# Optimization experiments

Hardware: AMD Instinct MI355X
Metric: run time of the kernel (lower is better)

Reference implementation:

```python
import jax, jax.numpy as jnp
import numpy as np

SEQ, B, V, E, H, L, S_SRC = 128, 32, 32000, 1024, 1024, 3, 64


def setup_inputs() -> dict:
    key = jax.random.key(0)
    ks = jax.random.split(key, 8)
    sc = 0.05
    return {
        "tokens": jax.random.randint(ks[0], (SEQ, B), 0, V),
        "emb_W": jax.random.normal(ks[1], (V, E), jnp.float32) * 0.1,
        "W_ih": jax.random.normal(ks[2], (L, 4 * H, E), jnp.float32) * sc,
        "W_hh": jax.random.normal(ks[3], (L, 4 * H, H), jnp.float32) * sc,
        "b_ih": jnp.zeros((L, 4 * H), jnp.float32),
        "b_hh": jnp.zeros((L, 4 * H), jnp.float32),
        "attn_Win": jax.random.normal(ks[4], (E, E), jnp.float32) * sc,
        "attn_Wout": jax.random.normal(ks[5], (E, 2 * E), jnp.float32) * sc,
        "final_b": jnp.zeros((V,), jnp.float32),
        "encoder_outs": jax.random.normal(ks[6], (S_SRC, B, E), jnp.float32),
        "h0": jnp.zeros((L, B, H), jnp.float32),
        "c0": jnp.zeros((L, B, H), jnp.float32),
    }


def reference(tokens, emb_W, W_ih, W_hh, b_ih, b_hh, attn_Win, attn_Wout,
              final_b, encoder_outs, h0, c0):
    # Eval mode: all dropouts (dropoute/i/h/out) are identity.
    emb = emb_W[tokens]                                  # [SEQ, B, E]
    ctx = jnp.transpose(encoder_outs, (1, 0, 2))         # [B, S_src, E]

    def lstm_cell(x, h, c, l):
        gates = x @ W_ih[l].T + b_ih[l] + h @ W_hh[l].T + b_hh[l]  # [B, 4H]
        i, f, g, o = jnp.split(gates, 4, axis=-1)        # torch order: i,f,g,o
        i, f, o = jax.nn.sigmoid(i), jax.nn.sigmoid(f), jax.nn.sigmoid(o)
        g = jnp.tanh(g)
        c_new = f * c + i * g
        return o * jnp.tanh(c_new), c_new

    def step(carry, x_t):
        h, c = carry                                     # each [L, B, H]
        hs, cs = [], []
        inp = x_t
        for l in range(L):
            h_new, c_new = lstm_cell(inp, h[l], c[l], l)
            hs.append(h_new)
            cs.append(c_new)
            inp = h_new                                  # dropouth is identity
        # SoftDotAttention on last layer hidden
        target = h_new @ attn_Win.T                      # [B, E]
        attn = jax.nn.softmax(jnp.einsum('bse,be->bs', ctx, target), axis=-1)
        wc = jnp.einsum('bs,bse->be', attn, ctx)         # weighted context
        h_tilde = jnp.tanh(jnp.concatenate([wc, h_new], axis=-1) @ attn_Wout.T)
        return (jnp.stack(hs), jnp.stack(cs)), h_tilde

    (_, _), outs = jax.lax.scan(step, (h0, c0), emb)     # outs: [SEQ, B, E]
    logits = outs @ emb_W.T + final_b                    # tied weights: [SEQ, B, V]
    return logits
```

## Files before the change

kernel.cpp:

```cpp
#include <hip/hip_runtime.h>
#include <cstdint>
#include <cstddef>

#define SEQ   128
#define BB    32
#define EE    1024
#define HH    1024
#define G4    4096
#define VV    32000
#define NROWS 4096

typedef _Float16 h16x8 __attribute__((ext_vector_type(8)));
typedef _Float16 h16x4 __attribute__((ext_vector_type(4)));
typedef float f32x4  __attribute__((ext_vector_type(4)));

#define AS_G(p) ((const __attribute__((address_space(1))) void*)(p))
#define AS_L(p) ((__attribute__((address_space(3))) void*)(p))

__device__ __forceinline__ float sigmf(float x) { return 1.0f / (1.0f + expf(-x)); }

#define OFF_SYNC    0ull
#define OFF_HFRAG   33024ull
#define OFF_EMB     426240ull
#define OFF_X0      8814848ull
#define OFF_WIH0    42369280ull
#define OFF_WP4     50757888ull
#define OFF_WP0     84312320ull
#define OFF_EMBW    92700928ull
#define OFF_WIN     158236928ull
#define OFF_WOUT    160334080ull
#define OFF_ENC     164528384ull
#define OFF_H2ALL   168722688ull
#define OFF_CONCAT  177111296ull
#define OFF_TARGET  193888512ull
#define OFF_HT      202277120ull
#define WS_NEEDED   210665728ull

__global__ __launch_bounds__(256) void k_conv(const float* __restrict__ s,
                                              _Float16* __restrict__ d, int n4) {
  int i = blockIdx.x * blockDim.x + threadIdx.x;
  int st = gridDim.x * blockDim.x;
  for (; i < n4; i += st) {
    float4 v = ((const float4*)s)[i];
    h16x4 o; o[0] = (_Float16)v.x; o[1] = (_Float16)v.y; o[2] = (_Float16)v.z; o[3] = (_Float16)v.w;
    ((h16x4*)d)[i] = o;
  }
}

__global__ __launch_bounds__(256) void k_gather(const int* __restrict__ tok,
                                                const float* __restrict__ embW,
                                                _Float16* __restrict__ emb) {
  int row = blockIdx.x;
  int t = tok[row];
  float4 v = ((const float4*)(embW + (size_t)t * EE))[threadIdx.x];
  h16x4 o; o[0] = (_Float16)v.x; o[1] = (_Float16)v.y; o[2] = (_Float16)v.z; o[3] = (_Float16)v.w;
  ((h16x4*)(emb + (size_t)row * EE))[threadIdx.x] = o;
}

__global__ __launch_bounds__(256) void k_packw4(const float* __restrict__ Wih,
                                                const float* __restrict__ Whh,
                                                _Float16* __restrict__ out) {
  int i = blockIdx.x * blockDim.x + threadIdx.x;
  int st = gridDim.x * blockDim.x;
  const int total = 256 * 65536;
  for (; i < total; i += st) {
    int w = i >> 16, rem = i & 65535;
    int mat = rem >> 14, jj = (rem >> 10) & 15, k = rem & 1023;
    int layer = 1 + (mat >> 1), isHH = mat & 1;
    int row = ((jj >> 2) << 10) + (w << 2) + (jj & 3);
    int ks = k ^ ((jj & 7) << 3);
    const float* src = (isHH ? Whh : Wih) + (size_t)layer * G4 * 1024 + (size_t)row * 1024 + ks;
    out[i] = (_Float16)(*src);
  }
}

__global__ __launch_bounds__(256) void k_packw0(const float* __restrict__ Whh,
                                                _Float16* __restrict__ out) {
  int i = blockIdx.x * blockDim.x + threadIdx.x;
  int st = gridDim.x * blockDim.x;
  const int total = 256 * 16384;
  for (; i < total; i += st) {
    int w = i >> 14, rem = i & 16383;
    int ks = rem >> 9, lane = (rem >> 3) & 63, e = rem & 7;
    int jj = lane & 15, q = lane >> 4;
    int row = ((jj >> 2) << 10) + (w << 2) + (jj & 3);
    int k = ks * 32 + q * 8 + e;
    out[i] = (_Float16)Whh[(size_t)row * 1024 + k];
  }
}

__global__ __launch_bounds__(256) void k_init(const float* __restrict__ h0,
                                              _Float16* __restrict__ hfrag,
                                              unsigned* __restrict__ sync) {
  int i = blockIdx.x * blockDim.x + threadIdx.x;
  if (i < 64 + 8192) sync[i] = 0u;
  if (i >= 3 * BB * HH) return;
  int l = i >> 15, rem = i & 32767;
  int b = rem >> 10, n = rem & 1023;
  int parI = (l == 1) ? 0 : 1;
  int tbb = b >> 4, ks = n >> 5, q = (n >> 3) & 3, e = n & 7;
  int lane2 = (b & 15) | (q << 4);
  hfrag[(size_t)(l * 2 + parI) * 32768 + ((size_t)(tbb * 32 + ks) * 64 + lane2) * 8 + e] =
      (_Float16)h0[i];
}

template <int EPI>
__global__ __launch_bounds__(256) void k_gemm(const _Float16* __restrict__ A,
                                              const _Float16* __restrict__ B,
                                              void* __restrict__ C, int M, int N, int K,
                                              const float* __restrict__ bias1,
                                              const float* __restrict__ bias2) {
  __shared__ _Float16 As[2][128 * 32];
  __shared__ _Float16 Bs[2][128 * 32];
  const int ntn = N / 128;
  const int tm = blockIdx.x / ntn, tn = blockIdx.x % ntn;
  const int tid = threadIdx.x, lane = tid & 63;
  const int wv = tid >> 6, wr = wv >> 1, wc = wv & 1;
  f32x4 acc[4][4] = {};

  auto stage = [&](int buf, int k0) {
#pragma unroll
    for (int i = 0; i < 2; ++i) {
      int eo = (i * 256 + tid) * 8;
      int r = eo >> 5, c = eo & 31;
      __builtin_amdgcn_global_load_lds(AS_G(A + (size_t)(tm * 128 + r) * K + k0 + c),
                                       AS_L(&As[buf][eo]), 16, 0, 0);
      __builtin_amdgcn_global_load_lds(AS_G(B + (size_t)(tn * 128 + r) * K + k0 + c),
                                       AS_L(&Bs[buf][eo]), 16, 0, 0);
    }
  };
  stage(0, 0);
  __syncthreads();
  const int nk = K / 32;
  for (int kt = 0; kt < nk; ++kt) {
    if (kt + 1 < nk) stage((kt + 1) & 1, (kt + 1) * 32);
    const int buf = kt & 1;
    h16x8 af[4], bfr[4];
#pragma unroll
    for (int mi = 0; mi < 4; ++mi)
      af[mi] = *(const h16x8*)&As[buf][(wr * 64 + mi * 16 + (lane & 15)) * 32 + (lane >> 4) * 8];
#pragma unroll
    for (int ni = 0; ni < 4; ++ni)
      bfr[ni] = *(const h16x8*)&Bs[buf][(wc * 64 + ni * 16 + (lane & 15)) * 32 + (lane >> 4) * 8];
#pragma unroll
    for (int mi = 0; mi < 4; ++mi)
#pragma unroll
      for (int ni = 0; ni < 4; ++ni)
        acc[mi][ni] = __builtin_amdgcn_mfma_f32_16x16x32_f16(af[mi], bfr[ni], acc[mi][ni], 0, 0, 0);
    __syncthreads();
  }
  const int rbase = tm * 128 + wr * 64;
  const int cbase = tn * 128 + wc * 64;
#pragma unroll
  for (int mi = 0; mi < 4; ++mi) {
#pragma unroll
    for (int ni = 0; ni < 4; ++ni) {
#pragma unroll
      for (int r = 0; r < 4; ++r) {
        int mm = rbase + mi * 16 + (lane >> 4) * 4 + r;
        int nn = cbase + ni * 16 + (lane & 15);
        float v = acc[mi][ni][r];
        if (EPI == 0) {
          ((float*)C)[(size_t)mm * N + nn] = v + bias1[nn];
        } else if (EPI == 1) {
          ((_Float16*)C)[(size_t)mm * N + nn] = (_Float16)v;
        } else if (EPI == 2) {
          ((_Float16*)C)[(size_t)mm * N + nn] = (_Float16)tanhf(v);
        } else {
          ((_Float16*)C)[(size_t)mm * N + nn] = (_Float16)(v + bias1[nn] + bias2[nn]);
        }
      }
    }
  }
}

__global__ __launch_bounds__(512) void k_recur(const _Float16* __restrict__ Wp4,
                                               const _Float16* __restrict__ Wp0,
                                               const _Float16* __restrict__ X0bf,
                                               _Float16* __restrict__ hfrag,
                                               _Float16* __restrict__ h2all,
                                               _Float16* __restrict__ concat,
                                               const float* __restrict__ bih,
                                               const float* __restrict__ bhh,
                                               const float* __restrict__ c0p,
                                               unsigned* __restrict__ sync) {
  extern __shared__ char lds[];
  _Float16* ldsW = (_Float16*)lds;
  float* redbuf = (float*)(lds + 131072);
  _Float16* hstage = (_Float16*)(lds + 131072);
  float* gbuf = (float*)(lds + 149504);
  unsigned* arrive = sync + 64;

  const int w = blockIdx.x;
  const int tid = threadIdx.x, lane = tid & 63, wv = tid >> 6;
  const int tb = wv & 1, kq = wv >> 1;
  const int row = (lane >> 4) * 4, col = lane & 15;

  for (int i = 0; i < 16; ++i) {
    int eo = (i * 512 + tid) * 8;
    *(h16x8*)&ldsW[eo] = *(const h16x8*)(Wp4 + (size_t)w * 65536 + eo);
  }
  h16x8 w0reg[8];
#pragma unroll
  for (int i = 0; i < 8; ++i)
    w0reg[i] = *(const h16x8*)(Wp0 + (size_t)w * 16384 + ((size_t)(kq * 8 + i) * 64 + lane) * 8);

  const int eb = tid >> 2, eni = tid & 3, en = w * 4 + eni;
  float c0r = 0.f, c1r = 0.f, c2r = 0.f;
  float b1r[4] = {0, 0, 0, 0}, b2r[4] = {0, 0, 0, 0};
  if (tid < 128) {
    c0r = c0p[0 * BB * HH + eb * HH + en];
    c1r = c0p[1 * BB * HH + eb * HH + en];
    c2r = c0p[2 * BB * HH + eb * HH + en];
#pragma unroll
    for (int g = 0; g < 4; ++g) {
      b1r[g] = bih[1 * G4 + g * 1024 + en] + bhh[1 * G4 + g * 1024 + en];
      b2r[g] = bih[2 * G4 + g * 1024 + en] + bhh[2 * G4 + g * 1024 + en];
    }
  }
  const int pk_l = tid >> 5, pk_r = tid & 31;
  const size_t pk_idx = ((size_t)(((pk_r >> 4) * 32 + (w >> 3)) * 64 + (pk_r & 15) +
                                  (((w >> 1) & 3) << 4))) * 8 + 4 * (w & 1);
  __syncthreads();

  for (int tau = 0; tau < 130; ++tau) {
    const int p = tau & 1;
    const _Float16* h0r = hfrag + (size_t)(0 + (1 - p)) * 32768;
    const _Float16* h1r = hfrag + (size_t)(2 + (1 - p)) * 32768;
    const _Float16* h2r = hfrag + (size_t)(4 + (1 - p)) * 32768;

    h16x8 a0[8], a1[8], a2[8];
#pragma unroll
    for (int i = 0; i < 8; ++i) {
      int ks = kq * 8 + i;
      size_t off = ((size_t)(tb * 32 + ks) * 64 + lane) * 8;
      a0[i] = *(const h16x8*)(h0r + off);
      a1[i] = *(const h16x8*)(h1r + off);
      a2[i] = *(const h16x8*)(h2r + off);
    }
    float xg0 = 0.f, xg1 = 0.f, xg2 = 0.f, xg3 = 0.f;
    if (tid < 128 && tau < 128) {
      size_t xb = ((size_t)(tau * BB + eb)) * G4 + en;
      xg0 = (float)X0bf[xb];        xg1 = (float)X0bf[xb + 1024];
      xg2 = (float)X0bf[xb + 2048]; xg3 = (float)X0bf[xb + 3072];
    }
    f32x4 acc0 = {}, acc1 = {}, acc2 = {};
#pragma unroll
    for (int i = 0; i < 8; ++i) {
      int ks = kq * 8 + i;
      int jj = lane & 15, q = lane >> 4;
      int kk = (ks * 32 + q * 8) ^ ((jj & 7) << 3);
      const h16x8 bw1i = *(const h16x8*)&ldsW[0 * 16384 + jj * 1024 + kk];
      const h16x8 bw1h = *(const h16x8*)&ldsW[1 * 16384 + jj * 1024 + kk];
      const h16x8 bw2i = *(const h16x8*)&ldsW[2 * 16384 + jj * 1024 + kk];
      const h16x8 bw2h = *(const h16x8*)&ldsW[3 * 16384 + jj * 1024 + kk];
      acc0 = __builtin_amdgcn_mfma_f32_16x16x32_f16(a0[i], w0reg[i], acc0, 0, 0, 0);
      acc1 = __builtin_amdgcn_mfma_f32_16x16x32_f16(a0[i], bw1i, acc1, 0, 0, 0);
      acc1 = __builtin_amdgcn_mfma_f32_16x16x32_f16(a1[i], bw1h, acc1, 0, 0, 0);
      acc2 = __builtin_amdgcn_mfma_f32_16x16x32_f16(a1[i], bw2i, acc2, 0, 0, 0);
      acc2 = __builtin_amdgcn_mfma_f32_16x16x32_f16(a2[i], bw2h, acc2, 0, 0, 0);
    }
    if (kq >= 1) {
      int s = kq - 1;
#pragma unroll
      for (int r = 0; r < 4; ++r) {
        redbuf[((0 * 3 + s) * 2 + tb) * 256 + (row + r) * 16 + col] = acc0[r];
        redbuf[((1 * 3 + s) * 2 + tb) * 256 + (row + r) * 16 + col] = acc1[r];
        redbuf[((2 * 3 + s) * 2 + tb) * 256 + (row + r) * 16 + col] = acc2[r];
      }
    }
    __syncthreads();
    if (kq == 0) {
#pragma unroll
      for (int r = 0; r < 4; ++r) {
        float v0 = acc0[r], v1 = acc1[r], v2 = acc2[r];
#pragma unroll
        for (int s = 0; s < 3; ++s) {
          v0 += redbuf[((0 * 3 + s) * 2 + tb) * 256 + (row + r) * 16 + col];
          v1 += redbuf[((1 * 3 + s) * 2 + tb) * 256 + (row + r) * 16 + col];
          v2 += redbuf[((2 * 3 + s) * 2 + tb) * 256 + (row + r) * 16 + col];
        }
        gbuf[(0 * 32 + tb * 16 + row + r) * 16 + col] = v0;
        gbuf[(1 * 32 + tb * 16 + row + r) * 16 + col] = v1;
        gbuf[(2 * 32 + tb * 16 + row + r) * 16 + col] = v2;
      }
    }
    __syncthreads();
    if (tid < 128) {
      if (tau < 128) {
        float gi = gbuf[(0 * 32 + eb) * 16 + eni] + xg0;
        float gf = gbuf[(0 * 32 + eb) * 16 + 4 + eni] + xg1;
        float gg = gbuf[(0 * 32 + eb) * 16 + 8 + eni] + xg2;
        float go = gbuf[(0 * 32 + eb) * 16 + 12 + eni] + xg3;
        c0r = sigmf(gf) * c0r + sigmf(gi) * tanhf(gg);
        hstage[0 * 128 + tid] = (_Float16)(sigmf(go) * tanhf(c0r));
      }
      if (tau >= 1 && tau < 129) {
        float gi = gbuf[(1 * 32 + eb) * 16 + eni] + b1r[0];
        float gf = gbuf[(1 * 32 + eb) * 16 + 4 + eni] + b1r[1];
        float gg = gbuf[(1 * 32 + eb) * 16 + 8 + eni] + b1r[2];
        float go = gbuf[(1 * 32 + eb) * 16 + 12 + eni] + b1r[3];
        c1r = sigmf(gf) * c1r + sigmf(gi) * tanhf(gg);
        hstage[1 * 128 + tid] = (_Float16)(sigmf(go) * tanhf(c1r));
      }
      if (tau >= 2) {
        float gi = gbuf[(2 * 32 + eb) * 16 + eni] + b2r[0];
        float gf = gbuf[(2 * 32 + eb) * 16 + 4 + eni] + b2r[1];
        float gg = gbuf[(2 * 32 + eb) * 16 + 8 + eni] + b2r[2];
        float go = gbuf[(2 * 32 + eb) * 16 + 12 + eni] + b2r[3];
        c2r = sigmf(gf) * c2r + sigmf(gi) * tanhf(gg);
        float h = sigmf(go) * tanhf(c2r);
        _Float16 hb = (_Float16)h;
        hstage[2 * 128 + tid] = hb;
        int t2 = tau - 2;
        h2all[(size_t)(t2 * BB + eb) * HH + en] = hb;
        concat[(size_t)(t2 * BB + eb) * 2048 + 1024 + en] = hb;
      }
    }
    __syncthreads();
    {
      bool act = (tid < 96) &&
                 ((pk_l == 0) ? (tau < 128)
                  : (pk_l == 1) ? (tau >= 1 && tau < 129) : (tau >= 2));
      if (act) {
        unsigned long long v = *(const unsigned long long*)&hstage[pk_l * 128 + pk_r * 4];
        __hip_atomic_store(
            (unsigned long long*)(hfrag + (size_t)(pk_l * 2 + p) * 32768 + pk_idx), v,
            __ATOMIC_RELAXED, __HIP_MEMORY_SCOPE_AGENT);
      }
      asm volatile("s_waitcnt vmcnt(0)" ::: "memory");
    }
    __syncthreads();
    if (tid == 0)
      __hip_atomic_store(&arrive[w * 32], (unsigned)(tau + 1), __ATOMIC_RELAXED,
                         __HIP_MEMORY_SCOPE_AGENT);
    if (tau < 129) {
      if (tid < 64) {
        for (;;) {
          bool ok = true;
#pragma unroll
          for (int j = 0; j < 4; ++j) {
            unsigned v = __hip_atomic_load(&arrive[(tid * 4 + j) * 32], __ATOMIC_RELAXED,
                                           __HIP_MEMORY_SCOPE_AGENT);
            ok &= (v >= (unsigned)(tau + 1));
          }
          if (__all(ok)) break;
          __builtin_amdgcn_s_sleep(1);
        }
        __builtin_amdgcn_fence(__ATOMIC_ACQUIRE, "agent");
      }
      __syncthreads();
    }
  }
}

__global__ __launch_bounds__(256) void k_attn(const _Float16* __restrict__ target,
                                              const _Float16* __restrict__ encb,
                                              _Float16* __restrict__ concat) {
  __shared__ float sc[64];
  __shared__ float att[64];
  int m = blockIdx.x, b = m & 31;
  int tid = threadIdx.x, lane = tid & 63, wv = tid >> 6;
  const h16x8* tp = (const h16x8*)(target + (size_t)m * EE + lane * 16);
  h16x8 tg0 = tp[0], tg1 = tp[1];
  for (int si = 0; si < 16; ++si) {
    int s = wv * 16 + si;
    const h16x8* ep = (const h16x8*)(encb + ((size_t)s * BB + b) * EE + lane * 16);
    h16x8 e0 = ep[0], e1 = ep[1];
    float a = 0.f;
#pragma unroll
    for (int j = 0; j < 8; ++j) a += (float)e0[j] * (float)tg0[j];
#pragma unroll
    for (int j = 0; j < 8; ++j) a += (float)e1[j] * (float)tg1[j];
#pragma unroll
    for (int off = 32; off >= 1; off >>= 1) a += __shfl_xor(a, off);
    if (lane == 0) sc[s] = a;
  }
  __syncthreads();
  if (wv == 0) {
    float v = sc[lane], mx = v;
#pragma unroll
    for (int off = 32; off >= 1; off >>= 1) mx = fmaxf(mx, __shfl_xor(mx, off));
    float e = expf(v - mx), sm = e;
#pragma unroll
    for (int off = 32; off >= 1; off >>= 1) sm += __shfl_xor(sm, off);
    att[lane] = e / sm;
  }
  __syncthreads();
  int e4 = tid * 4;
  float a0 = 0, a1 = 0, a2 = 0, a3 = 0;
  for (int s = 0; s < 64; ++s) {
    float wgt = att[s];
    h16x4 ev = *(const h16x4*)(encb + ((size_t)s * BB + b) * EE + e4);
    a0 += wgt * (float)ev[0]; a1 += wgt * (float)ev[1];
    a2 += wgt * (float)ev[2]; a3 += wgt * (float)ev[3];
  }
  h16x4 o; o[0] = (_Float16)a0; o[1] = (_Float16)a1; o[2] = (_Float16)a2; o[3] = (_Float16)a3;
  *(h16x4*)(concat + (size_t)m * 2048 + e4) = o;
}

extern "C" void kernel_launch(void* const* d_in, const int* in_sizes, int n_in,
                              void* d_out, int out_size, void* d_ws, size_t ws_size,
                              hipStream_t stream) {
  const int* tokens = (const int*)d_in[0];
  const float* embW = (const float*)d_in[1];
  const float* Wih = (const float*)d_in[2];
  const float* Whh = (const float*)d_in[3];
  const float* bih = (const float*)d_in[4];
  const float* bhh = (const float*)d_in[5];
  const float* Win = (const float*)d_in[6];
  const float* Wout = (const float*)d_in[7];
  const float* finalb = (const float*)d_in[8];
  const float* enc = (const float*)d_in[9];
  const float* h0 = (const float*)d_in[10];
  const float* c0 = (const float*)d_in[11];
  (void)in_sizes; (void)n_in; (void)out_size;
  if (ws_size < WS_NEEDED) return;

  char* ws = (char*)d_ws;
  unsigned* sync = (unsigned*)(ws + OFF_SYNC);
  _Float16* hfrag = (_Float16*)(ws + OFF_HFRAG);
  _Float16* emb = (_Float16*)(ws + OFF_EMB);
  _Float16* X0bf = (_Float16*)(ws + OFF_X0);
  _Float16* Wih0b = (_Float16*)(ws + OFF_WIH0);
  _Float16* Wp4 = (_Float16*)(ws + OFF_WP4);
  _Float16* Wp0 = (_Float16*)(ws + OFF_WP0);
  _Float16* embWb = (_Float16*)(ws + OFF_EMBW);
  _Float16* Winb = (_Float16*)(ws + OFF_WIN);
  _Float16* Woutb = (_Float16*)(ws + OFF_WOUT);
  _Float16* encb = (_Float16*)(ws + OFF_ENC);
  _Float16* h2all = (_Float16*)(ws + OFF_H2ALL);
  _Float16* concat = (_Float16*)(ws + OFF_CONCAT);
  _Float16* target = (_Float16*)(ws + OFF_TARGET);
  _Float16* ht = (_Float16*)(ws + OFF_HT);

  const unsigned LDSB = 155648;
  static int lds_set = 0;
  if (!lds_set) {
    hipFuncSetAttribute((const void*)k_recur, hipFuncAttributeMaxDynamicSharedMemorySize,
                        (int)LDSB);
    lds_set = 1;
  }

  k_conv<<<4096, 256, 0, stream>>>(embW, embWb, VV * EE / 4);
  k_conv<<<1024, 256, 0, stream>>>(Wih, Wih0b, G4 * EE / 4);
  k_conv<<<512, 256, 0, stream>>>(Win, Winb, EE * EE / 4);
  k_conv<<<512, 256, 0, stream>>>(Wout, Woutb, EE * 2048 / 4);
  k_conv<<<512, 256, 0, stream>>>(enc, encb, 64 * BB * EE / 4);
  k_gather<<<NROWS, 256, 0, stream>>>(tokens, embW, emb);
  k_packw4<<<8192, 256, 0, stream>>>(Wih, Whh, Wp4);
  k_packw0<<<4096, 256, 0, stream>>>(Whh, Wp0);
  k_init<<<384, 256, 0, stream>>>(h0, hfrag, sync);

  k_gemm<3><<<32 * 32, 256, 0, stream>>>(emb, Wih0b, X0bf, NROWS, G4, EE, bih, bhh);

  k_recur<<<256, 512, LDSB, stream>>>(Wp4, Wp0, X0bf, hfrag, h2all, concat,
                                      bih, bhh, c0, sync);

  k_gemm<1><<<32 * 8, 256, 0, stream>>>(h2all, Winb, target, NROWS, EE, EE, nullptr, nullptr);
  k_attn<<<NROWS, 256, 0, stream>>>(target, encb, concat);
  k_gemm<2><<<32 * 8, 256, 0, stream>>>(concat, Woutb, ht, NROWS, EE, 2048, nullptr, nullptr);

  k_gemm<0><<<32 * 250, 256, 0, stream>>>(ht, embWb, d_out, NROWS, VV, EE, finalb, nullptr);
}
```

Before: 1.724 ms.

## Use two-level hierarchical grid barrier in recurrent kernel and swizzle GEMM tiles

Replaces the flat grid barrier, where every workgroup polled all 256 arrival flags, with a two-level scheme. Leader workgroups each poll 32 arrivals and publish a summary flag, and every workgroup then polls only 8 summary flags. The hidden-state publish and barrier are folded into wave 0, which drops one block-wide sync per step. The GEMM block index is also permuted into 8-way interleaved order to change cache locality. The summary level adds a serial hop of latency per step.

```diff
diff --git a/kernel.cpp b/kernel.cpp
--- a/kernel.cpp
+++ b/kernel.cpp
@@ -20,21 +20,21 @@
 __device__ __forceinline__ float sigmf(float x) { return 1.0f / (1.0f + expf(-x)); }
 
 #define OFF_SYNC    0ull
-#define OFF_HFRAG   33024ull
-#define OFF_EMB     426240ull
-#define OFF_X0      8814848ull
-#define OFF_WIH0    42369280ull
-#define OFF_WP4     50757888ull
-#define OFF_WP0     84312320ull
-#define OFF_EMBW    92700928ull
-#define OFF_WIN     158236928ull
-#define OFF_WOUT    160334080ull
-#define OFF_ENC     164528384ull
-#define OFF_H2ALL   168722688ull
-#define OFF_CONCAT  177111296ull
-#define OFF_TARGET  193888512ull
-#define OFF_HT      202277120ull
-#define WS_NEEDED   210665728ull
+#define OFF_HFRAG   40960ull
+#define OFF_EMB     434176ull
+#define OFF_X0      8822784ull
+#define OFF_WIH0    42377216ull
+#define OFF_WP4     50765824ull
+#define OFF_WP0     84320256ull
+#define OFF_EMBW    92708864ull
+#define OFF_WIN     158244864ull
+#define OFF_WOUT    160342016ull
+#define OFF_ENC     164536320ull
+#define OFF_H2ALL   168730624ull
+#define OFF_CONCAT  177119232ull
+#define OFF_TARGET  193896448ull
+#define OFF_HT      202285056ull
+#define WS_NEEDED   210673664ull
 
 __global__ __launch_bounds__(256) void k_conv(const float* __restrict__ s,
                                               _Float16* __restrict__ d, int n4) {
@@ -93,7 +93,7 @@
                                               _Float16* __restrict__ hfrag,
                                               unsigned* __restrict__ sync) {
   int i = blockIdx.x * blockDim.x + threadIdx.x;
-  if (i < 64 + 8192) sync[i] = 0u;
+  if (i < 64 + 8192 + 256) sync[i] = 0u;
   if (i >= 3 * BB * HH) return;
   int l = i >> 15, rem = i & 32767;
   int b = rem >> 10, n = rem & 1023;
@@ -113,7 +113,9 @@
   __shared__ _Float16 As[2][128 * 32];
   __shared__ _Float16 Bs[2][128 * 32];
   const int ntn = N / 128;
-  const int tm = blockIdx.x / ntn, tn = blockIdx.x % ntn;
+  const int nwg = gridDim.x;
+  const int bid = (blockIdx.x & 7) * (nwg >> 3) + (blockIdx.x >> 3);
+  const int tm = bid / ntn, tn = bid % ntn;
   const int tid = threadIdx.x, lane = tid & 63;
   const int wv = tid >> 6, wr = wv >> 1, wc = wv & 1;
   f32x4 acc[4][4] = {};
@@ -190,6 +192,7 @@
   _Float16* hstage = (_Float16*)(lds + 131072);
   float* gbuf = (float*)(lds + 149504);
   unsigned* arrive = sync + 64;
+  unsigned* summary = sync + 64 + 8192;
 
   const int w = blockIdx.x;
   const int tid = threadIdx.x, lane = tid & 63, wv = tid >> 6;
@@ -218,8 +221,8 @@
       b2r[g] = bih[2 * G4 + g * 1024 + en] + bhh[2 * G4 + g * 1024 + en];
     }
   }
-  const int pk_l = tid >> 5, pk_r = tid & 31;
-  const size_t pk_idx = ((size_t)(((pk_r >> 4) * 32 + (w >> 3)) * 64 + (pk_r & 15) +
+  const int pr = lane & 31;
+  const size_t pk_idx = ((size_t)(((pr >> 4) * 32 + (w >> 3)) * 64 + (pr & 15) +
                                   (((w >> 1) & 3) << 4))) * 8 + 4 * (w & 1);
   __syncthreads();
 
@@ -318,39 +321,58 @@
       }
     }
     __syncthreads();
-    {
-      bool act = (tid < 96) &&
-                 ((pk_l == 0) ? (tau < 128)
-                  : (pk_l == 1) ? (tau >= 1 && tau < 129) : (tau >= 2));
-      if (act) {
-        unsigned long long v = *(const unsigned long long*)&hstage[pk_l * 128 + pk_r * 4];
-        __hip_atomic_store(
-            (unsigned long long*)(hfrag + (size_t)(pk_l * 2 + p) * 32768 + pk_idx), v,
-            __ATOMIC_RELAXED, __HIP_MEMORY_SCOPE_AGENT);
+    if (wv == 0) {
+      {
+        int l0 = lane >> 5;
+        bool act0 = (l0 == 0) ? (tau < 128) : (tau >= 1 && tau < 129);
+        if (act0) {
+          unsigned long long v = *(const unsigned long long*)&hstage[l0 * 128 + pr * 4];
+          __hip_atomic_store(
+              (unsigned long long*)(hfrag + (size_t)(l0 * 2 + p) * 32768 + pk_idx), v,
+              __ATOMIC_RELAXED, __HIP_MEMORY_SCOPE_AGENT);
+        }
+        if (lane < 32 && tau >= 2) {
+          unsigned long long v = *(const unsigned long long*)&hstage[2 * 128 + pr * 4];
+          __hip_atomic_store(
+              (unsigned long long*)(hfrag + (size_t)(4 + p) * 32768 + pk_idx), v,
+              __ATOMIC_RELAXED, __HIP_MEMORY_SCOPE_AGENT);
+        }
       }
       asm volatile("s_waitcnt vmcnt(0)" ::: "memory");
-    }
-    __syncthreads();
-    if (tid == 0)
-      __hip_atomic_store(&arrive[w * 32], (unsigned)(tau + 1), __ATOMIC_RELAXED,
-                         __HIP_MEMORY_SCOPE_AGENT);
-    if (tau < 129) {
-      if (tid < 64) {
+      if (lane == 0)
+        __hip_atomic_store(&arrive[w * 32], (unsigned)(tau + 1), __ATOMIC_RELAXED,
+                           __HIP_MEMORY_SCOPE_AGENT);
+      if (tau < 129) {
+        const unsigned tgt = (unsigned)(tau + 1);
+        if ((w & 31) == 0) {
+          for (;;) {
+            bool ok = true;
+            if (lane < 32) {
+              unsigned v = __hip_atomic_load(&arrive[(w + lane) * 32], __ATOMIC_RELAXED,
+                                             __HIP_MEMORY_SCOPE_AGENT);
+              ok = (v >= tgt);
+            }
+            if (__all(ok)) break;
+            __builtin_amdgcn_s_sleep(1);
+          }
+          if (lane == 0)
+            __hip_atomic_store(&summary[(w >> 5) * 32], tgt, __ATOMIC_RELAXED,
+                               __HIP_MEMORY_SCOPE_AGENT);
+        }
         for (;;) {
           bool ok = true;
-#pragma unroll
-          for (int j = 0; j < 4; ++j) {
-            unsigned v = __hip_atomic_load(&arrive[(tid * 4 + j) * 32], __ATOMIC_RELAXED,
+          if (lane < 8) {
+            unsigned v = __hip_atomic_load(&summary[lane * 32], __ATOMIC_RELAXED,
                                            __HIP_MEMORY_SCOPE_AGENT);
-            ok &= (v >= (unsigned)(tau + 1));
+            ok = (v >= tgt);
           }
           if (__all(ok)) break;
           __builtin_amdgcn_s_sleep(1);
         }
         __builtin_amdgcn_fence(__ATOMIC_ACQUIRE, "agent");
       }
-      __syncthreads();
-    }
+    }
+    __syncthreads();
   }
 }
 
```

Result: no change. 1.758 ms (+2.0%).
